# Optimization experiments

Hardware: AMD Instinct MI355X
Metric: run time of the kernel (lower is better)

Reference implementation:

```python
import jax, jax.numpy as jnp
import numpy as np

N_NODES = 50000
N_EDGES = 800000
N_GRAPHS = 64
HEADS = 8
HID = 16
D = HEADS * HID  # 128
N_CLASSES = 10
NEG_SLOPE = 0.2
N_LAYERS = 5


def setup_inputs() -> dict:
    key = jax.random.key(0)
    ks = jax.random.split(key, 12)
    x = jax.random.normal(ks[0], (N_NODES, D), dtype=jnp.float32)
    edge_index = jax.random.randint(ks[1], (2, N_EDGES), 0, N_NODES, dtype=jnp.int32)
    batch = jnp.sort(jax.random.randint(ks[2], (N_NODES,), 0, N_GRAPHS, dtype=jnp.int32))
    s = 1.0 / np.sqrt(D)
    # all 5 GATv2 layers share the same shapes (in = 8*hidden = 128); stack on axis 0
    Wl = jax.random.normal(ks[3], (N_LAYERS, D, D), dtype=jnp.float32) * s
    bl = jnp.zeros((N_LAYERS, D), dtype=jnp.float32)
    Wr = jax.random.normal(ks[4], (N_LAYERS, D, D), dtype=jnp.float32) * s
    br = jnp.zeros((N_LAYERS, D), dtype=jnp.float32)
    att = jax.random.normal(ks[5], (N_LAYERS, HEADS, HID), dtype=jnp.float32) * (1.0 / np.sqrt(HID))
    bias = jnp.zeros((N_LAYERS, D), dtype=jnp.float32)
    Wout = jax.random.normal(ks[6], (D, N_CLASSES), dtype=jnp.float32) * s
    bout = jnp.zeros((N_CLASSES,), dtype=jnp.float32)
    return {"x": x, "edge_index": edge_index, "batch": batch,
            "Wl": Wl, "bl": bl, "Wr": Wr, "br": br, "att": att, "bias": bias,
            "Wout": Wout, "bout": bout}


def gatv2_layer(x, src, dst, Wl, bl, Wr, br, att, bias):
    # x: [N, D_in]; returns [N, HEADS*HID]
    n = x.shape[0]
    xl = (x @ Wl + bl).reshape(n, HEADS, HID)   # source/message transform
    xr = (x @ Wr + br).reshape(n, HEADS, HID)   # target transform
    # GATv2 attention: att . leaky_relu(xl_j + xr_i) per edge, per head
    e = jax.nn.leaky_relu(xl[src] + xr[dst], NEG_SLOPE)          # [E, H, C]
    logits = jnp.einsum('ehc,hc->eh', e, att)                    # [E, H]
    # segment-softmax over incoming edges of each dst node
    m = jax.ops.segment_max(logits, dst, num_segments=n)         # [N, H]
    p = jnp.exp(logits - m[dst])
    denom = jax.ops.segment_sum(p, dst, num_segments=n)          # [N, H]
    alpha = p / denom[dst]                                       # [E, H]
    msg = xl[src] * alpha[:, :, None]                            # [E, H, C]
    out = jax.ops.segment_sum(msg, dst, num_segments=n)
    return out.reshape(n, HEADS * HID) + bias


def reference(x, edge_index, batch, Wl, bl, Wr, br, att, bias, Wout, bout):
    n = x.shape[0]
    # GATv2Conv(add_self_loops=True): append self loops to the edge list
    loops = jnp.arange(n, dtype=edge_index.dtype)
    src = jnp.concatenate([edge_index[0], loops])
    dst = jnp.concatenate([edge_index[1], loops])
    h = x
    for l in range(N_LAYERS):
        h = gatv2_layer(h, src, dst, Wl[l], bl[l], Wr[l], br[l], att[l], bias[l])
        h = jax.nn.elu(h)
    # global mean pool over graphs
    sums = jax.ops.segment_sum(h, batch, num_segments=N_GRAPHS)       # [G, D]
    counts = jax.ops.segment_sum(jnp.ones((n,), h.dtype), batch, num_segments=N_GRAPHS)
    pooled = sums / jnp.maximum(counts, 1.0)[:, None]
    logits = pooled @ Wout + bout
    return jax.nn.log_softmax(logits, axis=1)
```

## Files before the change

### kernel.cpp

```cpp
#include <hip/hip_runtime.h>
#include <hip/hip_bf16.h>
#include <math.h>

#define DD 128
#define HEADS 8
#define HID 16
#define NEG_SLOPE 0.2f
#define N_LAYERS 5
#define N_GRAPHS 64
#define N_CLASSES 10
#define NBINS 256
#define BIN_CAP 8192

typedef __bf16 bf16x8 __attribute__((ext_vector_type(8)));
typedef float f32x4 __attribute__((ext_vector_type(4)));
typedef float f32x2 __attribute__((ext_vector_type(2)));

__device__ __forceinline__ float bflo(unsigned u) { return __uint_as_float(u << 16); }
__device__ __forceinline__ float bfhi(unsigned u) { return __uint_as_float(u & 0xffff0000u); }
__device__ __forceinline__ float bf1(unsigned short us) { return __uint_as_float(((unsigned)us) << 16); }
__device__ __forceinline__ unsigned short f2bf(float f) {
    unsigned u = __float_as_uint(f);
    u += 0x7fffu + ((u >> 16) & 1u);
    return (unsigned short)(u >> 16);
}
__device__ __forceinline__ unsigned pack2bf(float a, float b) {
    return (unsigned)f2bf(a) | ((unsigned)f2bf(b) << 16);
}
__device__ __forceinline__ f32x2 unpk(unsigned u) {
    f32x2 r; r.x = bflo(u); r.y = bfhi(u); return r;
}

#define WCNT (N_LAYERS * 4 * 16 * 64)


__global__ void k_setup(const float* __restrict__ x, unsigned* __restrict__ xb,
                        const float* __restrict__ Wl, const float* __restrict__ Wr,
                        unsigned short* __restrict__ wB,
                        float* __restrict__ pooled, float* __restrict__ counts, int n2) {
    int id = blockIdx.x * 256 + threadIdx.x;
    if (id < n2) {
        float2 v = *(const float2*)(x + 2 * (size_t)id);
        xb[id] = pack2bf(v.x, v.y);
        return;
    }
    id -= n2;
    if (id < WCNT) {
        int lane = id & 63;
        int ntg  = (id >> 6) & 15;
        int ks   = (id >> 10) & 3;
        int l    = id >> 12;
        int q = lane >> 4, r = lane & 15;
        int n = ntg * 16 + r;
        const float* W = ((n < DD) ? Wl : Wr) + (size_t)l * DD * DD;
        int nn = n & (DD - 1);
        size_t off = (size_t)l * (4 * 16 * 64 * 8) + ((size_t)(ks * 16 + ntg) * 64 + lane) * 8;
        for (int j = 0; j < 8; ++j) {
            int k = ks * 32 + q * 8 + j;
            wB[off + j] = f2bf(W[(size_t)k * DD + nn]);
        }
        return;
    }
    id -= WCNT;
    if (id < N_GRAPHS * DD) { pooled[id] = 0.f; return; }
    id -= N_GRAPHS * DD;
    if (id < N_GRAPHS) counts[id] = 0.f;
}


__global__ __launch_bounds__(256) void k_bin_cnt(const int* __restrict__ ei,
        int* __restrict__ cnt, int n_edges, int n_total, int chunk,
        unsigned long long bin_mul) {
    __shared__ int hist[NBINS];
    int tid = threadIdx.x;
    hist[tid] = 0;
    __syncthreads();
    int beg = blockIdx.x * chunk;
    int end = beg + chunk; if (end > n_total) end = n_total;
    for (int e = beg + tid; e < end; e += 256) {
        int d = (e < n_edges) ? ei[n_edges + e] : (e - n_edges);
        int b = (int)(((unsigned long long)(unsigned)d * bin_mul) >> 32);
        atomicAdd(&hist[b], 1);
    }
    __syncthreads();
    cnt[tid * 256 + blockIdx.x] = hist[tid];
}

__global__ __launch_bounds__(256) void k_bin_scan(int* __restrict__ cnt, int* __restrict__ btot) {
    __shared__ int wsum[4];
    int b = blockIdx.x, t = threadIdx.x, wv = t >> 6, ln = t & 63;
    int v = cnt[b * 256 + t];
    int x = v;
#pragma unroll
    for (int ofs = 1; ofs < 64; ofs <<= 1) {
        int tt = __shfl_up(x, ofs);
        if (ln >= ofs) x += tt;
    }
    if (ln == 63) wsum[wv] = x;
    __syncthreads();
    int off = 0;
    for (int k = 0; k < wv; k++) off += wsum[k];
    int incl = off + x;
    cnt[b * 256 + t] = incl - v;
    if (t == 255) btot[b] = incl;
}

__global__ __launch_bounds__(256) void k_tot_scan(const int* __restrict__ btot,
        int* __restrict__ bin_start, int* __restrict__ row_ptr, int n_nodes) {
    __shared__ int wsum[4];
    int t = threadIdx.x, wv = t >> 6, ln = t & 63;
    int v = btot[t];
    int x = v;
#pragma unroll
    for (int ofs = 1; ofs < 64; ofs <<= 1) {
        int tt = __shfl_up(x, ofs);
        if (ln >= ofs) x += tt;
    }
    if (ln == 63) wsum[wv] = x;
    __syncthreads();
    int off = 0;
    for (int k = 0; k < wv; k++) off += wsum[k];
    int incl = off + x;
    bin_start[t] = incl - v;
    if (t == 255) { bin_start[256] = incl; row_ptr[n_nodes] = incl; }
}

__global__ __launch_bounds__(256) void k_bin_scatter(const int* __restrict__ ei,
        const int* __restrict__ cnt, const int* __restrict__ bin_start,
        unsigned* __restrict__ binned, int n_edges, int n_total, int chunk,
        unsigned long long bin_mul) {
    __shared__ int cur[NBINS];
    int tid = threadIdx.x;
    cur[tid] = bin_start[tid] + cnt[tid * 256 + blockIdx.x];
    __syncthreads();
    int beg = blockIdx.x * chunk;
    int end = beg + chunk; if (end > n_total) end = n_total;
    for (int e = beg + tid; e < end; e += 256) {
        int s, d;
        if (e < n_edges) { s = ei[e]; d = ei[n_edges + e]; }
        else { s = d = e - n_edges; }
        int b = (int)(((unsigned long long)(unsigned)d * bin_mul) >> 32);
        int pos = atomicAdd(&cur[b], 1);
        binned[pos] = (unsigned)s | ((unsigned)d << 16);
    }
}

__global__ __launch_bounds__(256) void k_bin_csr(const unsigned* __restrict__ binned,
        const int* __restrict__ bin_start, int* __restrict__ csr_src,
        int* __restrict__ row_ptr, int n_nodes, unsigned long long bin_mul) {
    __shared__ int sbuf[BIN_CAP];
    __shared__ int ldeg[256];
    __shared__ int wsum[4];
    int b = blockIdx.x, t = threadIdx.x, wv = t >> 6, ln = t & 63;
    int lo = (int)(((((unsigned long long)b) << 32) + bin_mul - 1) / bin_mul);
    int hi = (int)(((((unsigned long long)(b + 1)) << 32) + bin_mul - 1) / bin_mul);
    if (hi > n_nodes) hi = n_nodes;
    int estart = bin_start[b], eend = bin_start[b + 1];
    int ne = eend - estart;
    ldeg[t] = 0;
    __syncthreads();
    for (int k = t; k < ne; k += 256) {
        unsigned v = binned[estart + k];
        atomicAdd(&ldeg[(int)(v >> 16) - lo], 1);
    }
    __syncthreads();
    int vdeg = ldeg[t];
    int x = vdeg;
#pragma unroll
    for (int ofs = 1; ofs < 64; ofs <<= 1) {
        int tt = __shfl_up(x, ofs);
        if (ln >= ofs) x += tt;
    }
    if (ln == 63) wsum[wv] = x;
    __syncthreads();
    int off = 0;
    for (int k = 0; k < wv; k++) off += wsum[k];
    int excl = off + x - vdeg;
    if (lo + t < hi) row_ptr[lo + t] = estart + excl;
    __syncthreads();
    ldeg[t] = excl;
    __syncthreads();
    for (int k = t; k < ne; k += 256) {
        unsigned v = binned[estart + k];
        int pos = atomicAdd(&ldeg[(int)(v >> 16) - lo], 1);
        sbuf[pos] = (int)(v & 0xffffu);
    }
    __syncthreads();
    for (int k = t; k < ne; k += 256)
        csr_src[estart + k] = sbuf[k];
}


__global__ __launch_bounds__(256) void k_gemm_mfma(
    const unsigned short* __restrict__ in, const unsigned short* __restrict__ wB,
    const float* __restrict__ bl, const float* __restrict__ br,
    unsigned short* __restrict__ xl, unsigned short* __restrict__ xr, int n_nodes) {
    int w = threadIdx.x >> 6;
    int lane = threadIdx.x & 63;
    int q = lane >> 4, r = lane & 15;
    int blk = blockIdx.x;

    f32x4 acc[4][4] = {};
#pragma unroll
    for (int ks = 0; ks < 4; ++ks) {
        bf16x8 bh[4];
#pragma unroll
        for (int nt = 0; nt < 4; ++nt) {
            int ntg = w * 4 + nt;
            bh[nt] = *(const bf16x8*)(wB + ((size_t)(ks * 16 + ntg) * 64 + lane) * 8);
        }
        bf16x8 ah[4];
#pragma unroll
        for (int mt = 0; mt < 4; ++mt) {
            int node = blk * 64 + mt * 16 + r;
            if (node >= n_nodes) node = n_nodes - 1;
            ah[mt] = *(const bf16x8*)(in + (size_t)node * DD + ks * 32 + q * 8);
        }
#pragma unroll
        for (int mt = 0; mt < 4; ++mt)
#pragma unroll
            for (int nt = 0; nt < 4; ++nt)
                acc[mt][nt] = __builtin_amdgcn_mfma_f32_16x16x32_bf16(ah[mt], bh[nt], acc[mt][nt], 0, 0, 0);
    }
#pragma unroll
    for (int nt = 0; nt < 4; ++nt) {
        int col = w * 64 + nt * 16 + r;
        float bv = (col < DD) ? bl[col] : br[col - DD];
        unsigned short* dstbase = (col < DD) ? (xl + col) : (xr + (col - DD));
#pragma unroll
        for (int mt = 0; mt < 4; ++mt)
#pragma unroll
            for (int reg = 0; reg < 4; ++reg) {
                int node = blk * 64 + mt * 16 + q * 4 + reg;
                if (node < n_nodes)
                    dstbase[(size_t)node * DD] = f2bf(acc[mt][nt][reg] + bv);
            }
    }
}


__global__ __launch_bounds__(256) void k_node_agg(
    const unsigned short* __restrict__ xl, const unsigned short* __restrict__ xr,
    const int* __restrict__ row_ptr, const int* __restrict__ csr_src,
    const float* __restrict__ att, const float* __restrict__ bias,
    unsigned short* __restrict__ h_out, int n_nodes) {
    int wave = threadIdx.x >> 6;
    int lane = threadIdx.x & 63;
    int node = blockIdx.x * 4 + wave;
    if (node >= n_nodes) return;
    int grp = lane >> 4, sl = lane & 15;
    int beg = row_ptr[node], end = row_ptr[node + 1];

    uint4 xru = *(const uint4*)(xr + (size_t)node * DD + sl * 8);
    f32x2 xr0 = unpk(xru.x), xr1 = unpk(xru.y), xr2 = unpk(xru.z), xr3 = unpk(xru.w);
    f32x2 xs0 = xr0 * NEG_SLOPE, xs1 = xr1 * NEG_SLOPE, xs2 = xr2 * NEG_SLOPE, xs3 = xr3 * NEG_SLOPE;
    float4 atA = *(const float4*)(att + sl * 8);
    float4 atB = *(const float4*)(att + sl * 8 + 4);
    f32x2 at0, at1, at2, at3;
    at0.x = atA.x; at0.y = atA.y; at1.x = atA.z; at1.y = atA.w;
    at2.x = atB.x; at2.y = atB.y; at3.x = atB.z; at3.y = atB.w;

    float l = 0.f;
    f32x2 A0 = {0.f, 0.f}, A1 = {0.f, 0.f}, A2 = {0.f, 0.f}, A3 = {0.f, 0.f};

    int t0 = beg + grp;
    uint4 xu = make_uint4(0u, 0u, 0u, 0u);
    int sidx = 0;
    if (t0 < end) {
        int s = csr_src[t0];
        xu = *(const uint4*)(xl + (size_t)s * DD + sl * 8);
    }
    if (t0 + 4 < end) sidx = csr_src[t0 + 4];

    for (int t = t0; t < end; t += 4) {
        uint4 cur = xu;
        int snew = 0;
        if (t + 8 < end) snew = csr_src[t + 8];
        if (t + 4 < end) xu = *(const uint4*)(xl + (size_t)sidx * DD + sl * 8);
        sidx = snew;

        f32x2 x0 = unpk(cur.x), x1 = unpk(cur.y), x2 = unpk(cur.z), x3 = unpk(cur.w);
        f32x2 v0 = x0 + xr0, v1 = x1 + xr1, v2 = x2 + xr2, v3 = x3 + xr3;
        f32x2 w0 = x0 * NEG_SLOPE + xs0, w1 = x1 * NEG_SLOPE + xs1;
        f32x2 w2 = x2 * NEG_SLOPE + xs2, w3 = x3 * NEG_SLOPE + xs3;
        f32x2 lv0 = __builtin_elementwise_max(v0, w0);
        f32x2 lv1 = __builtin_elementwise_max(v1, w1);
        f32x2 lv2 = __builtin_elementwise_max(v2, w2);
        f32x2 lv3 = __builtin_elementwise_max(v3, w3);
        f32x2 d = lv0 * at0;
        d = lv1 * at1 + d;
        d = lv2 * at2 + d;
        d = lv3 * at3 + d;
        float lg = d.x + d.y;
        lg += __shfl_xor(lg, 1);
        float p = __expf(lg);
        l += p;
        f32x2 p2; p2.x = p; p2.y = p;
        A0 = x0 * p2 + A0;
        A1 = x1 * p2 + A1;
        A2 = x2 * p2 + A2;
        A3 = x3 * p2 + A3;
    }
    l += __shfl_xor(l, 16); l += __shfl_xor(l, 32);
    A0.x += __shfl_xor(A0.x, 16); A0.x += __shfl_xor(A0.x, 32);
    A0.y += __shfl_xor(A0.y, 16); A0.y += __shfl_xor(A0.y, 32);
    A1.x += __shfl_xor(A1.x, 16); A1.x += __shfl_xor(A1.x, 32);
    A1.y += __shfl_xor(A1.y, 16); A1.y += __shfl_xor(A1.y, 32);
    A2.x += __shfl_xor(A2.x, 16); A2.x += __shfl_xor(A2.x, 32);
    A2.y += __shfl_xor(A2.y, 16); A2.y += __shfl_xor(A2.y, 32);
    A3.x += __shfl_xor(A3.x, 16); A3.x += __shfl_xor(A3.x, 32);
    A3.y += __shfl_xor(A3.y, 16); A3.y += __shfl_xor(A3.y, 32);

    if (grp == 0) {
        float4 bvA = *(const float4*)(bias + sl * 8);
        float4 bvB = *(const float4*)(bias + sl * 8 + 4);
        float rl = 1.f / l;
        float o0 = A0.x * rl + bvA.x; o0 = o0 > 0.f ? o0 : __expf(o0) - 1.f;
        float o1 = A0.y * rl + bvA.y; o1 = o1 > 0.f ? o1 : __expf(o1) - 1.f;
        float o2 = A1.x * rl + bvA.z; o2 = o2 > 0.f ? o2 : __expf(o2) - 1.f;
        float o3 = A1.y * rl + bvA.w; o3 = o3 > 0.f ? o3 : __expf(o3) - 1.f;
        float o4 = A2.x * rl + bvB.x; o4 = o4 > 0.f ? o4 : __expf(o4) - 1.f;
        float o5 = A2.y * rl + bvB.y; o5 = o5 > 0.f ? o5 : __expf(o5) - 1.f;
        float o6 = A3.x * rl + bvB.z; o6 = o6 > 0.f ? o6 : __expf(o6) - 1.f;
        float o7 = A3.y * rl + bvB.w; o7 = o7 > 0.f ? o7 : __expf(o7) - 1.f;
        uint4 o;
        o.x = pack2bf(o0, o1); o.y = pack2bf(o2, o3);
        o.z = pack2bf(o4, o5); o.w = pack2bf(o6, o7);
        *(uint4*)(h_out + (size_t)node * DD + sl * 8) = o;
    }
}


__global__ void k_pool2(const unsigned short* __restrict__ h, const int* __restrict__ batch,
                        float* __restrict__ pooled, float* __restrict__ counts,
                        int n_nodes, int chunk) {
    int c = threadIdx.x;
    int beg = blockIdx.x * chunk;
    if (beg >= n_nodes) return;
    int end = beg + chunk; if (end > n_nodes) end = n_nodes;
    int cur = batch[beg];
    float acc = 0.f; int cnt = 0;
    for (int node = beg; node < end; ++node) {
        int g = batch[node];
        if (g != cur) {
            atomicAdd(&pooled[cur * DD + c], acc);
            if (c == 0) atomicAdd(&counts[cur], (float)cnt);
            acc = 0.f; cnt = 0; cur = g;
        }
        acc += bf1(h[(size_t)node * DD + c]);
        cnt++;
    }
    atomicAdd(&pooled[cur * DD + c], acc);
    if (c == 0) atomicAdd(&counts[cur], (float)cnt);
}

__global__ void k_final(const float* __restrict__ pooled, const float* __restrict__ counts,
                        const float* __restrict__ Wout, const float* __restrict__ bout,
                        float* __restrict__ out) {
    __shared__ float slog[N_GRAPHS * N_CLASSES];
    int t = threadIdx.x;
    int g = t / N_CLASSES, c = t % N_CLASSES;
    float cnt = fmaxf(counts[g], 1.f);
    float acc = bout[c];
    for (int k = 0; k < DD; k++)
        acc += (pooled[g * DD + k] / cnt) * Wout[k * N_CLASSES + c];
    slog[t] = acc;
    __syncthreads();
    float mx = -INFINITY;
    for (int j = 0; j < N_CLASSES; j++) mx = fmaxf(mx, slog[g * N_CLASSES + j]);
    float se = 0.f;
    for (int j = 0; j < N_CLASSES; j++) se += __expf(slog[g * N_CLASSES + j] - mx);
    out[t] = acc - mx - __logf(se);
}

extern "C" void kernel_launch(void* const* d_in, const int* in_sizes, int n_in,
                              void* d_out, int out_size, void* d_ws, size_t ws_size,
                              hipStream_t stream) {
    const float* x     = (const float*)d_in[0];
    const int*   ei    = (const int*)d_in[1];
    const int*   batch = (const int*)d_in[2];
    const float* Wl    = (const float*)d_in[3];
    const float* bl    = (const float*)d_in[4];
    const float* Wr    = (const float*)d_in[5];
    const float* br    = (const float*)d_in[6];
    const float* att   = (const float*)d_in[7];
    const float* bias  = (const float*)d_in[8];
    const float* Wout  = (const float*)d_in[9];
    const float* bout  = (const float*)d_in[10];
    float* out = (float*)d_out;

    int n_nodes = in_sizes[0] / DD;
    int n_edges = in_sizes[1] / 2;
    int n_total = n_edges + n_nodes;
    int ND = n_nodes * DD;

    const int WPL = 4 * 16 * 64 * 8;
    unsigned long long bin_mul = (((unsigned long long)NBINS) << 32) / (unsigned)n_nodes;

    unsigned short* hb  = (unsigned short*)d_ws;
    unsigned short* xb  = hb + (size_t)ND;
    unsigned short* xlb = xb + (size_t)ND;
    unsigned short* xrb = xlb + (size_t)ND;
    unsigned short* wB  = xrb + (size_t)ND;
    int*      cnt       = (int*)(wB + (size_t)N_LAYERS * WPL);
    int*      btot      = cnt + NBINS * 256;
    int*      bin_start = btot + NBINS;
    unsigned* binned    = (unsigned*)(bin_start + NBINS + 1);
    int*      csr_src   = (int*)(binned + n_total);
    int*      row_ptr   = csr_src + n_total;
    float*    pooled    = (float*)(row_ptr + n_nodes + 1);
    float*    counts    = pooled + N_GRAPHS * DD;

    dim3 b256(256);
    int gGemm = (n_nodes + 63) / 64;
    int gAgg  = (n_nodes + 3) / 4;
    int chunk = (n_total + 255) / 256;
    int poolBlocks = 1024;
    int poolChunk = (n_nodes + poolBlocks - 1) / poolBlocks;

    int n2 = ND / 2;
    int setupTotal = n2 + WCNT + N_GRAPHS * DD + N_GRAPHS;
    k_setup<<<(setupTotal + 255) / 256, b256, 0, stream>>>(x, (unsigned*)xb, Wl, Wr, wB,
                                                           pooled, counts, n2);
    k_bin_cnt<<<256, b256, 0, stream>>>(ei, cnt, n_edges, n_total, chunk, bin_mul);
    k_bin_scan<<<NBINS, b256, 0, stream>>>(cnt, btot);
    k_tot_scan<<<1, b256, 0, stream>>>(btot, bin_start, row_ptr, n_nodes);
    k_bin_scatter<<<256, b256, 0, stream>>>(ei, cnt, bin_start, binned, n_edges, n_total,
                                            chunk, bin_mul);
    k_bin_csr<<<NBINS, b256, 0, stream>>>(binned, bin_start, csr_src, row_ptr, n_nodes, bin_mul);

    for (int l = 0; l < N_LAYERS; l++) {
        const float* bl_l   = bl   + (size_t)l * DD;
        const float* br_l   = br   + (size_t)l * DD;
        const float* att_l  = att  + (size_t)l * HEADS * HID;
        const float* bias_l = bias + (size_t)l * DD;
        const unsigned short* in = (l == 0) ? xb : hb;

        k_gemm_mfma<<<gGemm, b256, 0, stream>>>(in, wB + (size_t)l * WPL, bl_l, br_l,
                                                xlb, xrb, n_nodes);
        k_node_agg<<<gAgg, b256, 0, stream>>>(xlb, xrb, row_ptr, csr_src, att_l, bias_l, hb, n_nodes);
    }

    k_pool2<<<poolBlocks, dim3(128), 0, stream>>>(hb, batch, pooled, counts, n_nodes, poolChunk);
    k_final<<<1, dim3(N_GRAPHS * N_CLASSES), 0, stream>>>(pooled, counts, Wout, bout, out);
}
```

Baseline: 501.0 us.

## Merge preprocessing kernels and deepen gather prefetch in node aggregation

Folds the bin-count histogram into the setup kernel. The total-bin scan now runs in the last block of the per-bin scan, found through an atomic done counter, and the final classifier runs in the last block of the pooling kernel. Together these cut kernel launches and the gaps between them. The aggregation loop now prefetches two neighbour rows ahead instead of one, to hide gather latency. In exchange it adds a memset for the done counters, uses threadfence-based last-block synchronisation, and raises register pressure in the aggregation kernel.

```diff
diff --git a/kernel.cpp b/kernel.cpp
--- a/kernel.cpp
+++ b/kernel.cpp
@@ -34,11 +34,30 @@
 #define WCNT (N_LAYERS * 4 * 16 * 64)
 
 
-__global__ void k_setup(const float* __restrict__ x, unsigned* __restrict__ xb,
-                        const float* __restrict__ Wl, const float* __restrict__ Wr,
-                        unsigned short* __restrict__ wB,
-                        float* __restrict__ pooled, float* __restrict__ counts, int n2) {
-    int id = blockIdx.x * 256 + threadIdx.x;
+__global__ __launch_bounds__(256) void k_setup_cnt(
+        const float* __restrict__ x, unsigned* __restrict__ xb,
+        const float* __restrict__ Wl, const float* __restrict__ Wr,
+        unsigned short* __restrict__ wB, float* __restrict__ pooled,
+        float* __restrict__ counts, const int* __restrict__ ei, int* __restrict__ cnt,
+        int n2, int n_edges, int n_total, int chunk, unsigned long long bin_mul) {
+    int blk = blockIdx.x;
+    if (blk < 256) {
+        __shared__ int hist[NBINS];
+        int tid = threadIdx.x;
+        hist[tid] = 0;
+        __syncthreads();
+        int beg = blk * chunk;
+        int end = beg + chunk; if (end > n_total) end = n_total;
+        for (int e = beg + tid; e < end; e += 256) {
+            int d = (e < n_edges) ? ei[n_edges + e] : (e - n_edges);
+            int b = (int)(((unsigned long long)(unsigned)d * bin_mul) >> 32);
+            atomicAdd(&hist[b], 1);
+        }
+        __syncthreads();
+        cnt[tid * 256 + blk] = hist[tid];
+        return;
+    }
+    int id = (blk - 256) * 256 + threadIdx.x;
     if (id < n2) {
         float2 v = *(const float2*)(x + 2 * (size_t)id);
         xb[id] = pack2bf(v.x, v.y);
@@ -68,26 +87,11 @@
 }
 
 
-__global__ __launch_bounds__(256) void k_bin_cnt(const int* __restrict__ ei,
-        int* __restrict__ cnt, int n_edges, int n_total, int chunk,
-        unsigned long long bin_mul) {
-    __shared__ int hist[NBINS];
-    int tid = threadIdx.x;
-    hist[tid] = 0;
-    __syncthreads();
-    int beg = blockIdx.x * chunk;
-    int end = beg + chunk; if (end > n_total) end = n_total;
-    for (int e = beg + tid; e < end; e += 256) {
-        int d = (e < n_edges) ? ei[n_edges + e] : (e - n_edges);
-        int b = (int)(((unsigned long long)(unsigned)d * bin_mul) >> 32);
-        atomicAdd(&hist[b], 1);
-    }
-    __syncthreads();
-    cnt[tid * 256 + blockIdx.x] = hist[tid];
-}
-
-__global__ __launch_bounds__(256) void k_bin_scan(int* __restrict__ cnt, int* __restrict__ btot) {
+__global__ __launch_bounds__(256) void k_bin_scan(int* __restrict__ cnt,
+        int* __restrict__ btot, int* __restrict__ bin_start, int* __restrict__ row_ptr,
+        int* __restrict__ done, int n_nodes) {
     __shared__ int wsum[4];
+    __shared__ int amLast;
     int b = blockIdx.x, t = threadIdx.x, wv = t >> 6, ln = t & 63;
     int v = cnt[b * 256 + t];
     int x = v;
@@ -103,26 +107,26 @@
     int incl = off + x;
     cnt[b * 256 + t] = incl - v;
     if (t == 255) btot[b] = incl;
-}
-
-__global__ __launch_bounds__(256) void k_tot_scan(const int* __restrict__ btot,
-        int* __restrict__ bin_start, int* __restrict__ row_ptr, int n_nodes) {
-    __shared__ int wsum[4];
-    int t = threadIdx.x, wv = t >> 6, ln = t & 63;
-    int v = btot[t];
-    int x = v;
+    __threadfence();
+    if (t == 0) amLast = (atomicAdd(done, 1) == NBINS - 1);
+    __syncthreads();
+    if (!amLast) return;
+    __threadfence();
+    int v2 = btot[t];
+    int x2 = v2;
 #pragma unroll
     for (int ofs = 1; ofs < 64; ofs <<= 1) {
-        int tt = __shfl_up(x, ofs);
-        if (ln >= ofs) x += tt;
-    }
-    if (ln == 63) wsum[wv] = x;
-    __syncthreads();
-    int off = 0;
-    for (int k = 0; k < wv; k++) off += wsum[k];
-    int incl = off + x;
-    bin_start[t] = incl - v;
-    if (t == 255) { bin_start[256] = incl; row_ptr[n_nodes] = incl; }
+        int tt = __shfl_up(x2, ofs);
+        if (ln >= ofs) x2 += tt;
+    }
+    __syncthreads();
+    if (ln == 63) wsum[wv] = x2;
+    __syncthreads();
+    int off2 = 0;
+    for (int k = 0; k < wv; k++) off2 += wsum[k];
+    int incl2 = off2 + x2;
+    bin_start[t] = incl2 - v2;
+    if (t == 255) { bin_start[256] = incl2; row_ptr[n_nodes] = incl2; }
 }
 
 __global__ __launch_bounds__(256) void k_bin_scatter(const int* __restrict__ ei,
@@ -264,20 +268,24 @@
     f32x2 A0 = {0.f, 0.f}, A1 = {0.f, 0.f}, A2 = {0.f, 0.f}, A3 = {0.f, 0.f};
 
     int t0 = beg + grp;
-    uint4 xu = make_uint4(0u, 0u, 0u, 0u);
-    int sidx = 0;
+    uint4 rA = make_uint4(0u, 0u, 0u, 0u);
+    uint4 rB = make_uint4(0u, 0u, 0u, 0u);
+    int sN = 0;
     if (t0 < end) {
         int s = csr_src[t0];
-        xu = *(const uint4*)(xl + (size_t)s * DD + sl * 8);
-    }
-    if (t0 + 4 < end) sidx = csr_src[t0 + 4];
+        rA = *(const uint4*)(xl + (size_t)s * DD + sl * 8);
+    }
+    if (t0 + 4 < end) {
+        int s = csr_src[t0 + 4];
+        rB = *(const uint4*)(xl + (size_t)s * DD + sl * 8);
+    }
+    if (t0 + 8 < end) sN = csr_src[t0 + 8];
 
     for (int t = t0; t < end; t += 4) {
-        uint4 cur = xu;
-        int snew = 0;
-        if (t + 8 < end) snew = csr_src[t + 8];
-        if (t + 4 < end) xu = *(const uint4*)(xl + (size_t)sidx * DD + sl * 8);
-        sidx = snew;
+        uint4 cur = rA;
+        rA = rB;
+        if (t + 8 < end) rB = *(const uint4*)(xl + (size_t)sN * DD + sl * 8);
+        if (t + 12 < end) sN = csr_src[t + 12];
 
         f32x2 x0 = unpk(cur.x), x1 = unpk(cur.y), x2 = unpk(cur.z), x3 = unpk(cur.w);
         f32x2 v0 = x0 + xr0, v1 = x1 + xr1, v2 = x2 + xr2, v3 = x3 + xr3;
@@ -331,46 +339,56 @@
 }
 
 
-__global__ void k_pool2(const unsigned short* __restrict__ h, const int* __restrict__ batch,
-                        float* __restrict__ pooled, float* __restrict__ counts,
-                        int n_nodes, int chunk) {
+__global__ __launch_bounds__(128) void k_pool_final(
+        const unsigned short* __restrict__ h, const int* __restrict__ batch,
+        float* __restrict__ pooled, float* __restrict__ counts,
+        const float* __restrict__ Wout, const float* __restrict__ bout,
+        float* __restrict__ out, int* __restrict__ done,
+        int n_nodes, int chunk, int nblocks) {
     int c = threadIdx.x;
     int beg = blockIdx.x * chunk;
-    if (beg >= n_nodes) return;
-    int end = beg + chunk; if (end > n_nodes) end = n_nodes;
-    int cur = batch[beg];
-    float acc = 0.f; int cnt = 0;
-    for (int node = beg; node < end; ++node) {
-        int g = batch[node];
-        if (g != cur) {
-            atomicAdd(&pooled[cur * DD + c], acc);
-            if (c == 0) atomicAdd(&counts[cur], (float)cnt);
-            acc = 0.f; cnt = 0; cur = g;
+    if (beg < n_nodes) {
+        int end = beg + chunk; if (end > n_nodes) end = n_nodes;
+        int cur = batch[beg];
+        float acc = 0.f; int cnt = 0;
+        for (int node = beg; node < end; ++node) {
+            int g = batch[node];
+            if (g != cur) {
+                atomicAdd(&pooled[cur * DD + c], acc);
+                if (c == 0) atomicAdd(&counts[cur], (float)cnt);
+                acc = 0.f; cnt = 0; cur = g;
+            }
+            acc += bf1(h[(size_t)node * DD + c]);
+            cnt++;
         }
-        acc += bf1(h[(size_t)node * DD + c]);
-        cnt++;
-    }
-    atomicAdd(&pooled[cur * DD + c], acc);
-    if (c == 0) atomicAdd(&counts[cur], (float)cnt);
-}
-
-__global__ void k_final(const float* __restrict__ pooled, const float* __restrict__ counts,
-                        const float* __restrict__ Wout, const float* __restrict__ bout,
-                        float* __restrict__ out) {
+        atomicAdd(&pooled[cur * DD + c], acc);
+        if (c == 0) atomicAdd(&counts[cur], (float)cnt);
+    }
+    __threadfence();
+    __shared__ int amLast;
+    if (c == 0) amLast = (atomicAdd(done, 1) == nblocks - 1);
+    __syncthreads();
+    if (!amLast) return;
+    __threadfence();
     __shared__ float slog[N_GRAPHS * N_CLASSES];
-    int t = threadIdx.x;
-    int g = t / N_CLASSES, c = t % N_CLASSES;
-    float cnt = fmaxf(counts[g], 1.f);
-    float acc = bout[c];
-    for (int k = 0; k < DD; k++)
-        acc += (pooled[g * DD + k] / cnt) * Wout[k * N_CLASSES + c];
-    slog[t] = acc;
-    __syncthreads();
-    float mx = -INFINITY;
-    for (int j = 0; j < N_CLASSES; j++) mx = fmaxf(mx, slog[g * N_CLASSES + j]);
-    float se = 0.f;
-    for (int j = 0; j < N_CLASSES; j++) se += __expf(slog[g * N_CLASSES + j] - mx);
-    out[t] = acc - mx - __logf(se);
+    for (int i = c; i < N_GRAPHS * N_CLASSES; i += 128) {
+        int g = i / N_CLASSES, cl = i % N_CLASSES;
+        float cntv = fmaxf(counts[g], 1.f);
+        float acc = bout[cl];
+        for (int k = 0; k < DD; k++)
+            acc += (pooled[g * DD + k] / cntv) * Wout[k * N_CLASSES + cl];
+        slog[i] = acc;
+    }
+    __syncthreads();
+    for (int g = c; g < N_GRAPHS; g += 128) {
+        float mx = -INFINITY;
+        for (int j = 0; j < N_CLASSES; j++) mx = fmaxf(mx, slog[g * N_CLASSES + j]);
+        float se = 0.f;
+        for (int j = 0; j < N_CLASSES; j++) se += __expf(slog[g * N_CLASSES + j] - mx);
+        float lse = mx + __logf(se);
+        for (int j = 0; j < N_CLASSES; j++)
+            out[g * N_CLASSES + j] = slog[g * N_CLASSES + j] - lse;
+    }
 }
 
 extern "C" void kernel_launch(void* const* d_in, const int* in_sizes, int n_in,
@@ -397,7 +415,8 @@
     const int WPL = 4 * 16 * 64 * 8;
     unsigned long long bin_mul = (((unsigned long long)NBINS) << 32) / (unsigned)n_nodes;
 
-    unsigned short* hb  = (unsigned short*)d_ws;
+    int* done           = (int*)d_ws;
+    unsigned short* hb  = (unsigned short*)((char*)d_ws + 256);
     unsigned short* xb  = hb + (size_t)ND;
     unsigned short* xlb = xb + (size_t)ND;
     unsigned short* xrb = xlb + (size_t)ND;
@@ -420,11 +439,12 @@
 
     int n2 = ND / 2;
     int setupTotal = n2 + WCNT + N_GRAPHS * DD + N_GRAPHS;
-    k_setup<<<(setupTotal + 255) / 256, b256, 0, stream>>>(x, (unsigned*)xb, Wl, Wr, wB,
-                                                           pooled, counts, n2);
-    k_bin_cnt<<<256, b256, 0, stream>>>(ei, cnt, n_edges, n_total, chunk, bin_mul);
-    k_bin_scan<<<NBINS, b256, 0, stream>>>(cnt, btot);
-    k_tot_scan<<<1, b256, 0, stream>>>(btot, bin_start, row_ptr, n_nodes);
+    int gSetup = 256 + (setupTotal + 255) / 256;
+
+    hipMemsetAsync(d_ws, 0, 256, stream);
+    k_setup_cnt<<<gSetup, b256, 0, stream>>>(x, (unsigned*)xb, Wl, Wr, wB, pooled, counts,
+                                             ei, cnt, n2, n_edges, n_total, chunk, bin_mul);
+    k_bin_scan<<<NBINS, b256, 0, stream>>>(cnt, btot, bin_start, row_ptr, &done[0], n_nodes);
     k_bin_scatter<<<256, b256, 0, stream>>>(ei, cnt, bin_start, binned, n_edges, n_total,
                                             chunk, bin_mul);
     k_bin_csr<<<NBINS, b256, 0, stream>>>(binned, bin_start, csr_src, row_ptr, n_nodes, bin_mul);
@@ -441,6 +461,6 @@
         k_node_agg<<<gAgg, b256, 0, stream>>>(xlb, xrb, row_ptr, csr_src, att_l, bias_l, hb, n_nodes);
     }
 
-    k_pool2<<<poolBlocks, dim3(128), 0, stream>>>(hb, batch, pooled, counts, n_nodes, poolChunk);
-    k_final<<<1, dim3(N_GRAPHS * N_CLASSES), 0, stream>>>(pooled, counts, Wout, bout, out);
-}
+    k_pool_final<<<poolBlocks, dim3(128), 0, stream>>>(hb, batch, pooled, counts, Wout, bout,
+                                                       out, &done[1], n_nodes, poolChunk, poolBlocks);
+}
```

Result: slower. 576.1 us (+15.0%).

## Remap node aggregation to 8 lanes per node with full-head ownership

Applied to the files above, without the earlier changes.

The aggregation kernel now assigns 8 threads per node, each owning one full head (16 channels), so a wave handles 8 nodes instead of one node split across four edge groups. This removes the per-edge cross-lane shuffle for the logit and the final cross-group reductions, and processes edges serially per node with a two-deep prefetch. In exchange each thread holds twice the registers and walks all edges alone, so per-node latency grows and lanes in a wave diverge when neighbour counts differ.

```diff
diff --git a/kernel.cpp b/kernel.cpp
--- a/kernel.cpp
+++ b/kernel.cpp
@@ -244,90 +244,95 @@
     const int* __restrict__ row_ptr, const int* __restrict__ csr_src,
     const float* __restrict__ att, const float* __restrict__ bias,
     unsigned short* __restrict__ h_out, int n_nodes) {
-    int wave = threadIdx.x >> 6;
-    int lane = threadIdx.x & 63;
-    int node = blockIdx.x * 4 + wave;
+    int tid = threadIdx.x;
+    int grp = tid >> 3;
+    int j   = tid & 7;
+    int node = blockIdx.x * 32 + grp;
     if (node >= n_nodes) return;
-    int grp = lane >> 4, sl = lane & 15;
     int beg = row_ptr[node], end = row_ptr[node + 1];
 
-    uint4 xru = *(const uint4*)(xr + (size_t)node * DD + sl * 8);
-    f32x2 xr0 = unpk(xru.x), xr1 = unpk(xru.y), xr2 = unpk(xru.z), xr3 = unpk(xru.w);
-    f32x2 xs0 = xr0 * NEG_SLOPE, xs1 = xr1 * NEG_SLOPE, xs2 = xr2 * NEG_SLOPE, xs3 = xr3 * NEG_SLOPE;
-    float4 atA = *(const float4*)(att + sl * 8);
-    float4 atB = *(const float4*)(att + sl * 8 + 4);
-    f32x2 at0, at1, at2, at3;
-    at0.x = atA.x; at0.y = atA.y; at1.x = atA.z; at1.y = atA.w;
-    at2.x = atB.x; at2.y = atB.y; at3.x = atB.z; at3.y = atB.w;
+    const unsigned short* xrp = xr + (size_t)node * DD + j * 16;
+    uint4 xa = *(const uint4*)xrp;
+    uint4 xc = *(const uint4*)(xrp + 8);
+    f32x2 q0 = unpk(xa.x), q1 = unpk(xa.y), q2 = unpk(xa.z), q3 = unpk(xa.w);
+    f32x2 q4 = unpk(xc.x), q5 = unpk(xc.y), q6 = unpk(xc.z), q7 = unpk(xc.w);
+    const float* ap = att + j * 16;
+    f32x2 at0 = *(const f32x2*)(ap +  0), at1 = *(const f32x2*)(ap +  2);
+    f32x2 at2 = *(const f32x2*)(ap +  4), at3 = *(const f32x2*)(ap +  6);
+    f32x2 at4 = *(const f32x2*)(ap +  8), at5 = *(const f32x2*)(ap + 10);
+    f32x2 at6 = *(const f32x2*)(ap + 12), at7 = *(const f32x2*)(ap + 14);
 
     float l = 0.f;
-    f32x2 A0 = {0.f, 0.f}, A1 = {0.f, 0.f}, A2 = {0.f, 0.f}, A3 = {0.f, 0.f};
-
-    int t0 = beg + grp;
-    uint4 xu = make_uint4(0u, 0u, 0u, 0u);
-    int sidx = 0;
-    if (t0 < end) {
-        int s = csr_src[t0];
-        xu = *(const uint4*)(xl + (size_t)s * DD + sl * 8);
-    }
-    if (t0 + 4 < end) sidx = csr_src[t0 + 4];
-
-    for (int t = t0; t < end; t += 4) {
-        uint4 cur = xu;
-        int snew = 0;
-        if (t + 8 < end) snew = csr_src[t + 8];
-        if (t + 4 < end) xu = *(const uint4*)(xl + (size_t)sidx * DD + sl * 8);
-        sidx = snew;
-
-        f32x2 x0 = unpk(cur.x), x1 = unpk(cur.y), x2 = unpk(cur.z), x3 = unpk(cur.w);
-        f32x2 v0 = x0 + xr0, v1 = x1 + xr1, v2 = x2 + xr2, v3 = x3 + xr3;
-        f32x2 w0 = x0 * NEG_SLOPE + xs0, w1 = x1 * NEG_SLOPE + xs1;
-        f32x2 w2 = x2 * NEG_SLOPE + xs2, w3 = x3 * NEG_SLOPE + xs3;
-        f32x2 lv0 = __builtin_elementwise_max(v0, w0);
-        f32x2 lv1 = __builtin_elementwise_max(v1, w1);
-        f32x2 lv2 = __builtin_elementwise_max(v2, w2);
-        f32x2 lv3 = __builtin_elementwise_max(v3, w3);
-        f32x2 d = lv0 * at0;
-        d = lv1 * at1 + d;
-        d = lv2 * at2 + d;
-        d = lv3 * at3 + d;
+    f32x2 A0 = {0.f,0.f}, A1 = {0.f,0.f}, A2 = {0.f,0.f}, A3 = {0.f,0.f};
+    f32x2 A4 = {0.f,0.f}, A5 = {0.f,0.f}, A6 = {0.f,0.f}, A7 = {0.f,0.f};
+
+    uint4 rA0, rA1, rB0, rB1;
+    rB0 = rB1 = make_uint4(0u, 0u, 0u, 0u);
+    int sN = 0;
+    {
+        const unsigned short* p = xl + (size_t)csr_src[beg] * DD + j * 16;
+        rA0 = *(const uint4*)p; rA1 = *(const uint4*)(p + 8);
+    }
+    if (beg + 1 < end) {
+        const unsigned short* p = xl + (size_t)csr_src[beg + 1] * DD + j * 16;
+        rB0 = *(const uint4*)p; rB1 = *(const uint4*)(p + 8);
+    }
+    if (beg + 2 < end) sN = csr_src[beg + 2];
+
+    for (int t = beg; t < end; ++t) {
+        uint4 c0 = rA0, c1 = rA1;
+        rA0 = rB0; rA1 = rB1;
+        if (t + 2 < end) {
+            const unsigned short* p = xl + (size_t)sN * DD + j * 16;
+            rB0 = *(const uint4*)p; rB1 = *(const uint4*)(p + 8);
+        }
+        if (t + 3 < end) sN = csr_src[t + 3];
+
+        f32x2 x0 = unpk(c0.x), x1 = unpk(c0.y), x2 = unpk(c0.z), x3 = unpk(c0.w);
+        f32x2 x4 = unpk(c1.x), x5 = unpk(c1.y), x6 = unpk(c1.z), x7 = unpk(c1.w);
+        f32x2 v0 = x0 + q0, v1 = x1 + q1, v2 = x2 + q2, v3 = x3 + q3;
+        f32x2 v4 = x4 + q4, v5 = x5 + q5, v6 = x6 + q6, v7 = x7 + q7;
+        f32x2 m0 = __builtin_elementwise_max(v0, v0 * NEG_SLOPE);
+        f32x2 m1 = __builtin_elementwise_max(v1, v1 * NEG_SLOPE);
+        f32x2 m2 = __builtin_elementwise_max(v2, v2 * NEG_SLOPE);
+        f32x2 m3 = __builtin_elementwise_max(v3, v3 * NEG_SLOPE);
+        f32x2 m4 = __builtin_elementwise_max(v4, v4 * NEG_SLOPE);
+        f32x2 m5 = __builtin_elementwise_max(v5, v5 * NEG_SLOPE);
+        f32x2 m6 = __builtin_elementwise_max(v6, v6 * NEG_SLOPE);
+        f32x2 m7 = __builtin_elementwise_max(v7, v7 * NEG_SLOPE);
+        f32x2 d = m0 * at0;
+        d = m1 * at1 + d; d = m2 * at2 + d; d = m3 * at3 + d;
+        d = m4 * at4 + d; d = m5 * at5 + d; d = m6 * at6 + d; d = m7 * at7 + d;
         float lg = d.x + d.y;
-        lg += __shfl_xor(lg, 1);
         float p = __expf(lg);
         l += p;
         f32x2 p2; p2.x = p; p2.y = p;
-        A0 = x0 * p2 + A0;
-        A1 = x1 * p2 + A1;
-        A2 = x2 * p2 + A2;
-        A3 = x3 * p2 + A3;
-    }
-    l += __shfl_xor(l, 16); l += __shfl_xor(l, 32);
-    A0.x += __shfl_xor(A0.x, 16); A0.x += __shfl_xor(A0.x, 32);
-    A0.y += __shfl_xor(A0.y, 16); A0.y += __shfl_xor(A0.y, 32);
-    A1.x += __shfl_xor(A1.x, 16); A1.x += __shfl_xor(A1.x, 32);
-    A1.y += __shfl_xor(A1.y, 16); A1.y += __shfl_xor(A1.y, 32);
-    A2.x += __shfl_xor(A2.x, 16); A2.x += __shfl_xor(A2.x, 32);
-    A2.y += __shfl_xor(A2.y, 16); A2.y += __shfl_xor(A2.y, 32);
-    A3.x += __shfl_xor(A3.x, 16); A3.x += __shfl_xor(A3.x, 32);
-    A3.y += __shfl_xor(A3.y, 16); A3.y += __shfl_xor(A3.y, 32);
-
-    if (grp == 0) {
-        float4 bvA = *(const float4*)(bias + sl * 8);
-        float4 bvB = *(const float4*)(bias + sl * 8 + 4);
-        float rl = 1.f / l;
-        float o0 = A0.x * rl + bvA.x; o0 = o0 > 0.f ? o0 : __expf(o0) - 1.f;
-        float o1 = A0.y * rl + bvA.y; o1 = o1 > 0.f ? o1 : __expf(o1) - 1.f;
-        float o2 = A1.x * rl + bvA.z; o2 = o2 > 0.f ? o2 : __expf(o2) - 1.f;
-        float o3 = A1.y * rl + bvA.w; o3 = o3 > 0.f ? o3 : __expf(o3) - 1.f;
-        float o4 = A2.x * rl + bvB.x; o4 = o4 > 0.f ? o4 : __expf(o4) - 1.f;
-        float o5 = A2.y * rl + bvB.y; o5 = o5 > 0.f ? o5 : __expf(o5) - 1.f;
-        float o6 = A3.x * rl + bvB.z; o6 = o6 > 0.f ? o6 : __expf(o6) - 1.f;
-        float o7 = A3.y * rl + bvB.w; o7 = o7 > 0.f ? o7 : __expf(o7) - 1.f;
-        uint4 o;
-        o.x = pack2bf(o0, o1); o.y = pack2bf(o2, o3);
-        o.z = pack2bf(o4, o5); o.w = pack2bf(o6, o7);
-        *(uint4*)(h_out + (size_t)node * DD + sl * 8) = o;
-    }
+        A0 = x0 * p2 + A0; A1 = x1 * p2 + A1; A2 = x2 * p2 + A2; A3 = x3 * p2 + A3;
+        A4 = x4 * p2 + A4; A5 = x5 * p2 + A5; A6 = x6 * p2 + A6; A7 = x7 * p2 + A7;
+    }
+
+    float rl = 1.f / l;
+    const float* bp = bias + j * 16;
+    f32x2 b0 = *(const f32x2*)(bp +  0), b1 = *(const f32x2*)(bp +  2);
+    f32x2 b2 = *(const f32x2*)(bp +  4), b3 = *(const f32x2*)(bp +  6);
+    f32x2 b4 = *(const f32x2*)(bp +  8), b5 = *(const f32x2*)(bp + 10);
+    f32x2 b6 = *(const f32x2*)(bp + 12), b7 = *(const f32x2*)(bp + 14);
+#define ELU1(z) ((z) > 0.f ? (z) : __expf(z) - 1.f)
+    f32x2 rl2; rl2.x = rl; rl2.y = rl;
+    f32x2 o0 = A0 * rl2 + b0, o1 = A1 * rl2 + b1, o2 = A2 * rl2 + b2, o3 = A3 * rl2 + b3;
+    f32x2 o4 = A4 * rl2 + b4, o5 = A5 * rl2 + b5, o6 = A6 * rl2 + b6, o7 = A7 * rl2 + b7;
+    uint4 O1, O2;
+    O1.x = pack2bf(ELU1(o0.x), ELU1(o0.y));
+    O1.y = pack2bf(ELU1(o1.x), ELU1(o1.y));
+    O1.z = pack2bf(ELU1(o2.x), ELU1(o2.y));
+    O1.w = pack2bf(ELU1(o3.x), ELU1(o3.y));
+    O2.x = pack2bf(ELU1(o4.x), ELU1(o4.y));
+    O2.y = pack2bf(ELU1(o5.x), ELU1(o5.y));
+    O2.z = pack2bf(ELU1(o6.x), ELU1(o6.y));
+    O2.w = pack2bf(ELU1(o7.x), ELU1(o7.y));
+    unsigned short* op = h_out + (size_t)node * DD + j * 16;
+    *(uint4*)op = O1;
+    *(uint4*)(op + 8) = O2;
 }
 
 
@@ -413,7 +418,7 @@
 
     dim3 b256(256);
     int gGemm = (n_nodes + 63) / 64;
-    int gAgg  = (n_nodes + 3) / 4;
+    int gAgg  = (n_nodes + 31) / 32;
     int chunk = (n_total + 255) / 256;
     int poolBlocks = 1024;
     int poolChunk = (n_nodes + poolBlocks - 1) / poolBlocks;
```

New measurement: 502.6 us. Within noise of the previous version (+0.3%).
